# Kernel tuning notes

Hardware: AMD Instinct MI355X
Metric: run time of the kernel (lower is better)

The kernel has to match this reference:

```python
import jax, jax.numpy as jnp
import numpy as np

N_NODES = 100000
N_EDGES = 3200000
OUT_FEATURES = 128


def setup_inputs() -> dict:
    key = jax.random.key(0)
    k1, k2, k3, k4, k5 = jax.random.split(key, 5)
    edge_row = jax.random.randint(k1, (N_EDGES,), 0, N_NODES, dtype=jnp.int32)
    edge_col = jax.random.randint(k2, (N_EDGES,), 0, N_NODES, dtype=jnp.int32)
    edge_val = jax.random.uniform(k3, (N_EDGES,), dtype=jnp.float32)
    stdv = 1.0 / np.sqrt(OUT_FEATURES)
    weight = jax.random.uniform(k4, (N_NODES, OUT_FEATURES), minval=-stdv, maxval=stdv, dtype=jnp.float32)
    bias = jax.random.uniform(k5, (OUT_FEATURES,), minval=-stdv, maxval=stdv, dtype=jnp.float32)
    return {"edge_row": edge_row, "edge_col": edge_col, "edge_val": edge_val,
            "weight": weight, "bias": bias}


def reference(edge_row, edge_col, edge_val, weight, bias):
    # SpMM: out = adj @ weight, adj given in COO (row, col, val), shape [N, N]
    n_nodes = weight.shape[0]
    gathered = edge_val[:, None] * weight[edge_col]            # [E, F]
    out = jax.ops.segment_sum(gathered, edge_row, num_segments=n_nodes)  # [N, F]
    return out + bias
```

## Files before the change

### kernel.cpp

```cpp
#include <hip/hip_runtime.h>

#define F 128
#define RB 64
#define RB_SHIFT 6
#define CAP 4096
#define SCH 4096
#define PT3 1024
#define EPT3 (SCH / PT3)
#define NSEG 8
#define COL_BITS 17
#define COL_MASK 0x1FFFF
#define MAXNB 2048

__global__ __launch_bounds__(256) void cvt_chist_kernel(
    const float4* __restrict__ w4, uint* __restrict__ wq32, float* __restrict__ scales,
    int total4, const int* __restrict__ rows, int* __restrict__ cntmat, int n_edges,
    int nb, int nchunks) {
    if ((int)blockIdx.x < nchunks) {
        __shared__ int h[MAXNB];
        int c = blockIdx.x, t = threadIdx.x;
        for (int i = t; i < nb; i += 256) h[i] = 0;
        __syncthreads();
        int e0 = c * SCH, e1 = min(e0 + SCH, n_edges);
        if (e1 - e0 == SCH) {
            const int4* r4 = (const int4*)(rows + e0);
#pragma unroll
            for (int k = 0; k < 4; k++) {
                int4 rv = r4[k * 256 + t];
                atomicAdd(&h[rv.x >> RB_SHIFT], 1);
                atomicAdd(&h[rv.y >> RB_SHIFT], 1);
                atomicAdd(&h[rv.z >> RB_SHIFT], 1);
                atomicAdd(&h[rv.w >> RB_SHIFT], 1);
            }
        } else {
            for (int e = e0 + t; e < e1; e += 256) atomicAdd(&h[rows[e] >> RB_SHIFT], 1);
        }
        __syncthreads();
        for (int i = t; i < nb; i += 256) cntmat[(size_t)c * nb + i] = h[i];
    } else {
        int idx = (blockIdx.x - nchunks) * 256 + threadIdx.x;
        if (idx >= total4) return;
        float4 f = w4[idx];
        float m = fmaxf(fmaxf(fabsf(f.x), fabsf(f.y)), fmaxf(fabsf(f.z), fabsf(f.w)));
#pragma unroll
        for (int off = 1; off <= 16; off <<= 1) m = fmaxf(m, __shfl_xor(m, off));
        float inv = m > 0.f ? 127.f / m : 0.f;
        int q0 = (int)rintf(f.x * inv);
        int q1 = (int)rintf(f.y * inv);
        int q2 = (int)rintf(f.z * inv);
        int q3 = (int)rintf(f.w * inv);
        wq32[idx] = (q0 & 0xFF) | ((q1 & 0xFF) << 8) | ((q2 & 0xFF) << 16) |
                    ((q3 & 0xFF) << 24);
        if ((idx & 31) == 0) scales[idx >> 5] = m * (1.f / 127.f);
    }
}

__global__ __launch_bounds__(256) void scanA_kernel(int* __restrict__ cntmat,
                                                    int* __restrict__ segsum,
                                                    int nb, int nchunks) {
    int b = blockIdx.x * 256 + threadIdx.x;
    if (b >= nb) return;
    int sg = blockIdx.y;
    int cps = (nchunks + NSEG - 1) / NSEG;
    int c0 = sg * cps, c1 = min(c0 + cps, nchunks);
    int run = 0;
#pragma unroll 4
    for (int c = c0; c < c1; c++) {
        int v = cntmat[(size_t)c * nb + b];
        cntmat[(size_t)c * nb + b] = run;
        run += v;
    }
    segsum[sg * nb + b] = run;
}

__global__ void scanBC_kernel(int* __restrict__ segsum, int* __restrict__ boffs, int nb) {
    __shared__ int lds[1024];
    int t = threadIdx.x;
    int per = (nb + 1023) / 1024;
    int base = t * per;
    int cnt[2] = {0, 0};
    int s = 0;
    for (int i = 0; i < per && i < 2; i++) {
        int b = base + i;
        int run = 0;
        if (b < nb) {
            for (int sg = 0; sg < NSEG; sg++) {
                int v = segsum[sg * nb + b];
                segsum[sg * nb + b] = run;
                run += v;
            }
        }
        cnt[i] = run;
        s += run;
    }
    lds[t] = s;
    __syncthreads();
    for (int off = 1; off < 1024; off <<= 1) {
        int a = (t >= off) ? lds[t - off] : 0;
        __syncthreads();
        lds[t] += a;
        __syncthreads();
    }
    int excl = lds[t] - s;
    for (int i = 0; i < per && i < 2; i++) {
        int b = base + i;
        if (b < nb) {
            boffs[b] = excl;
            excl += cnt[i];
        }
    }
    if (t == 1023) boffs[nb] = lds[1023];
}

__global__ __launch_bounds__(PT3) void scatter_kernel(
    const int* __restrict__ rows, const int* __restrict__ cols,
    const float* __restrict__ vals, const float* __restrict__ scales,
    const int* __restrict__ boffs, const int* __restrict__ segsum,
    const int* __restrict__ cntmat, int2* __restrict__ epk, int n_edges, int nb,
    int nchunks) {
    __shared__ int relc[MAXNB];
    __shared__ int hist[MAXNB];
    __shared__ int lcur[MAXNB];
    __shared__ int2 buf[SCH];
    __shared__ ushort sbkt[SCH];
    __shared__ int wsum[PT3 / 64], wbase[PT3 / 64];
    int t = threadIdx.x;
    int lane = t & 63, w = t >> 6;
    int cps = (nchunks + NSEG - 1) / NSEG;
    int c = blockIdx.x;

    int e0 = c * SCH, e1 = min(e0 + SCH, n_edges);
    int cnt = e1 - e0;
    int sg = c / cps;

    for (int i = t; i < nb; i += PT3) {
        relc[i] = boffs[i] + segsum[sg * nb + i] + cntmat[(size_t)c * nb + i];
        hist[i] = 0;
    }
    __syncthreads();

    int er[EPT3], ec[EPT3];
    float ev[EPT3];
    int eb = e0 + (t << 2);
    if (eb + 4 <= e1) {
        int4 rv = *(const int4*)(rows + eb);
        int4 cv = *(const int4*)(cols + eb);
        float4 vv = *(const float4*)(vals + eb);
        er[0] = rv.x; er[1] = rv.y; er[2] = rv.z; er[3] = rv.w;
        ec[0] = cv.x; ec[1] = cv.y; ec[2] = cv.z; ec[3] = cv.w;
        ev[0] = vv.x * scales[ec[0]];
        ev[1] = vv.y * scales[ec[1]];
        ev[2] = vv.z * scales[ec[2]];
        ev[3] = vv.w * scales[ec[3]];
#pragma unroll
        for (int k = 0; k < 4; k++) atomicAdd(&hist[er[k] >> RB_SHIFT], 1);
    } else {
#pragma unroll
        for (int k = 0; k < 4; k++) {
            int e = eb + k;
            if (e < e1) {
                er[k] = rows[e];
                ec[k] = cols[e];
                ev[k] = vals[e] * scales[ec[k]];
                atomicAdd(&hist[er[k] >> RB_SHIFT], 1);
            }
        }
    }
    __syncthreads();

    int b0 = t << 1;
    int h0 = (b0 + 0 < nb) ? hist[b0 + 0] : 0;
    int h1 = (b0 + 1 < nb) ? hist[b0 + 1] : 0;
    int psum = h0 + h1;
    int v = psum;
#pragma unroll
    for (int off = 1; off < 64; off <<= 1) {
        int a = __shfl_up(v, off);
        if (lane >= off) v += a;
    }
    if (lane == 63) wsum[w] = v;
    __syncthreads();
    if (t == 0) {
        int run = 0;
        for (int i = 0; i < PT3 / 64; i++) {
            wbase[i] = run;
            run += wsum[i];
        }
    }
    __syncthreads();
    int excl = v - psum + wbase[w];
    if (b0 + 0 < nb) { lcur[b0 + 0] = excl; relc[b0 + 0] -= excl; }
    excl += h0;
    if (b0 + 1 < nb) { lcur[b0 + 1] = excl; relc[b0 + 1] -= excl; }
    __syncthreads();

#pragma unroll
    for (int k = 0; k < EPT3; k++) {
        int e = eb + k;
        if (e < e1) {
            int b = er[k] >> RB_SHIFT;
            int p = atomicAdd(&lcur[b], 1);
            buf[p] = make_int2(ec[k] | ((er[k] & (RB - 1)) << COL_BITS),
                               __float_as_int(ev[k]));
            sbkt[p] = (ushort)b;
        }
    }
    __syncthreads();

    for (int i = t; i < cnt; i += PT3) epk[relc[sbkt[i]] + i] = buf[i];
}

__global__ __launch_bounds__(512, 8) void sortacc_kernel(
    const int* __restrict__ boffs, const int2* __restrict__ epk,
    const ushort* __restrict__ wq, const float* __restrict__ bias,
    float* __restrict__ out, int n_nodes) {
    __shared__ int2 buf[CAP];
    __shared__ int hist[RB], lstart[RB], lcur[RB];
    int b = blockIdx.x;
    int s = boffs[b];
    int cnt = boffs[b + 1] - s;
    int row0 = b << RB_SHIFT;
    int t = threadIdx.x;
    int lane = t & 63, w = t >> 6;
    float2 bb = ((const float2*)bias)[lane];

#define DEQX(u) ((float)(int)(signed char)((u) & 0xFF))
#define DEQY(u) ((float)((int)(short)(u) >> 8))
#define WOFF(px) ((((uint)(px) & COL_MASK) << 6) | (uint)lane)

    if (cnt <= CAP) {
        if (t < RB) hist[t] = 0;
        __syncthreads();
        int2 r0, r1, r2, r3, r4, r5, r6, r7;
#define LOADK(rk, k)                                                     \
        {                                                                \
            int i = t + (k)*512;                                         \
            if (i < cnt) {                                               \
                rk = epk[s + i];                                         \
                atomicAdd(&hist[(unsigned)rk.x >> COL_BITS], 1);         \
            }                                                            \
        }
        LOADK(r0, 0) LOADK(r1, 1) LOADK(r2, 2) LOADK(r3, 3)
        LOADK(r4, 4) LOADK(r5, 5) LOADK(r6, 6) LOADK(r7, 7)
#undef LOADK
        __syncthreads();
        if (w == 0) {
            int hv = hist[lane];
            int v = hv;
#pragma unroll
            for (int off = 1; off < 64; off <<= 1) {
                int a = __shfl_up(v, off);
                if (lane >= off) v += a;
            }
            lstart[lane] = v - hv;
            lcur[lane] = v - hv;
        }
        __syncthreads();
#define SCATK(rk, k)                                                         \
        {                                                                    \
            int i = t + (k)*512;                                             \
            if (i < cnt) {                                                   \
                int p = atomicAdd(&lcur[(unsigned)rk.x >> COL_BITS], 1);     \
                buf[p] = make_int2((int)(((uint)rk.x & COL_MASK) << 6), rk.y);\
            }                                                                \
        }
        SCATK(r0, 0) SCATK(r1, 1) SCATK(r2, 2) SCATK(r3, 3)
        SCATK(r4, 4) SCATK(r5, 5) SCATK(r6, 6) SCATK(r7, 7)
#undef SCATK
        __syncthreads();

        for (int j = 0; j < 8; j++) {
            int rl = w * 8 + j;
            int gr = row0 + rl;
            if (gr >= n_nodes) break;
            int e = lstart[rl];
            int end = e + hist[rl];
            float ax = 0.f, ay = 0.f;
            for (; e + 12 <= end; e += 12) {
                int2 p0 = buf[e],     p1 = buf[e + 1], p2 = buf[e + 2];
                int2 p3 = buf[e + 3], p4 = buf[e + 4], p5 = buf[e + 5];
                int2 p6 = buf[e + 6], p7 = buf[e + 7], p8 = buf[e + 8];
                int2 p9 = buf[e + 9], pa = buf[e + 10], pb = buf[e + 11];
                uint u0 = wq[(uint)p0.x + lane];
                uint u1 = wq[(uint)p1.x + lane];
                uint u2 = wq[(uint)p2.x + lane];
                uint u3 = wq[(uint)p3.x + lane];
                uint u4 = wq[(uint)p4.x + lane];
                uint u5 = wq[(uint)p5.x + lane];
                uint u6 = wq[(uint)p6.x + lane];
                uint u7 = wq[(uint)p7.x + lane];
                uint u8 = wq[(uint)p8.x + lane];
                uint u9 = wq[(uint)p9.x + lane];
                uint ua = wq[(uint)pa.x + lane];
                uint ub = wq[(uint)pb.x + lane];
                float v0 = __int_as_float(p0.y), v1 = __int_as_float(p1.y);
                float v2 = __int_as_float(p2.y), v3 = __int_as_float(p3.y);
                float v4 = __int_as_float(p4.y), v5 = __int_as_float(p5.y);
                float v6 = __int_as_float(p6.y), v7 = __int_as_float(p7.y);
                float v8 = __int_as_float(p8.y), v9 = __int_as_float(p9.y);
                float va = __int_as_float(pa.y), vb = __int_as_float(pb.y);
                ax += v0 * DEQX(u0) + v1 * DEQX(u1) + v2 * DEQX(u2) + v3 * DEQX(u3) +
                      v4 * DEQX(u4) + v5 * DEQX(u5) + v6 * DEQX(u6) + v7 * DEQX(u7) +
                      v8 * DEQX(u8) + v9 * DEQX(u9) + va * DEQX(ua) + vb * DEQX(ub);
                ay += v0 * DEQY(u0) + v1 * DEQY(u1) + v2 * DEQY(u2) + v3 * DEQY(u3) +
                      v4 * DEQY(u4) + v5 * DEQY(u5) + v6 * DEQY(u6) + v7 * DEQY(u7) +
                      v8 * DEQY(u8) + v9 * DEQY(u9) + va * DEQY(ua) + vb * DEQY(ub);
            }
            for (; e + 4 <= end; e += 4) {
                int2 p0 = buf[e], p1 = buf[e + 1], p2 = buf[e + 2], p3 = buf[e + 3];
                uint u0 = wq[(uint)p0.x + lane];
                uint u1 = wq[(uint)p1.x + lane];
                uint u2 = wq[(uint)p2.x + lane];
                uint u3 = wq[(uint)p3.x + lane];
                float v0 = __int_as_float(p0.y), v1 = __int_as_float(p1.y);
                float v2 = __int_as_float(p2.y), v3 = __int_as_float(p3.y);
                ax += v0 * DEQX(u0) + v1 * DEQX(u1) + v2 * DEQX(u2) + v3 * DEQX(u3);
                ay += v0 * DEQY(u0) + v1 * DEQY(u1) + v2 * DEQY(u2) + v3 * DEQY(u3);
            }
            for (; e < end; ++e) {
                int2 pk = buf[e];
                uint u = wq[(uint)pk.x + lane];
                float v = __int_as_float(pk.y);
                ax += v * DEQX(u);
                ay += v * DEQY(u);
            }
            ((float2*)(out + (size_t)gr * F))[lane] = make_float2(ax + bb.x, ay + bb.y);
        }
    } else {
        for (int j = 0; j < 8; j++) {
            int rl = w * 8 + j;
            int gr = row0 + rl;
            if (gr >= n_nodes) break;
            float ax = 0.f, ay = 0.f;
            for (int e = s; e < s + cnt; ++e) {
                int2 pk = epk[e];
                if ((int)((unsigned)pk.x >> COL_BITS) == rl) {
                    uint u = wq[WOFF(pk.x)];
                    float v = __int_as_float(pk.y);
                    ax += v * DEQX(u);
                    ay += v * DEQY(u);
                }
            }
            ((float2*)(out + (size_t)gr * F))[lane] = make_float2(ax + bb.x, ay + bb.y);
        }
    }
#undef DEQX
#undef DEQY
#undef WOFF
}

__global__ void init_out_kernel(float* __restrict__ out, const float* __restrict__ bias,
                                int n_nodes) {
    const float4* b4 = (const float4*)bias;
    float4* o4 = (float4*)out;
    int total = n_nodes * (F / 4);
    for (int i = blockIdx.x * blockDim.x + threadIdx.x; i < total;
         i += gridDim.x * blockDim.x)
        o4[i] = b4[i & (F / 4 - 1)];
}

__global__ void edge_scatter_kernel(const int* __restrict__ rows,
                                    const int* __restrict__ cols,
                                    const float* __restrict__ vals,
                                    const float* __restrict__ weight,
                                    float* __restrict__ out, int n_edges) {
    int e = (blockIdx.x * blockDim.x + threadIdx.x) >> 6;
    if (e >= n_edges) return;
    int lane = threadIdx.x & 63;
    float2 w = ((const float2*)(weight + (size_t)cols[e] * F))[lane];
    float val = vals[e];
    float* o = out + (size_t)rows[e] * F + lane * 2;
    unsafeAtomicAdd(o, val * w.x);
    unsafeAtomicAdd(o + 1, val * w.y);
}

extern "C" void kernel_launch(void* const* d_in, const int* in_sizes, int n_in,
                              void* d_out, int out_size, void* d_ws, size_t ws_size,
                              hipStream_t stream) {
    const int*   rows   = (const int*)d_in[0];
    const int*   cols   = (const int*)d_in[1];
    const float* vals   = (const float*)d_in[2];
    const float* weight = (const float*)d_in[3];
    const float* bias   = (const float*)d_in[4];
    float* out = (float*)d_out;

    int n_edges = in_sizes[0];
    int n_nodes = out_size / F;
    int nb = (n_nodes + RB - 1) / RB;
    int nchunks = (n_edges + SCH - 1) / SCH;

    size_t head_ints  = ((size_t)nb + 2) & ~(size_t)1;
    size_t epk_off    = head_ints * 4;
    size_t scales_off = epk_off + (size_t)n_edges * 8;
    size_t wq_off     = (scales_off + (size_t)n_nodes * 4 + 255) & ~(size_t)255;
    size_t mat_off    = (wq_off + (size_t)n_nodes * F + 255) & ~(size_t)255;
    size_t seg_off    = mat_off + (size_t)nchunks * nb * 4;
    size_t need       = seg_off + (size_t)NSEG * nb * 4;

    if (ws_size < need || n_nodes > (1 << COL_BITS) || nb > MAXNB) {
        init_out_kernel<<<2048, 256, 0, stream>>>(out, bias, n_nodes);
        int grid = (n_edges + 3) / 4;
        edge_scatter_kernel<<<grid, 256, 0, stream>>>(rows, cols, vals, weight, out,
                                                      n_edges);
        return;
    }

    int* boffs    = (int*)d_ws;
    int2* epk     = (int2*)((char*)d_ws + epk_off);
    float* scales = (float*)((char*)d_ws + scales_off);
    ushort* wq    = (ushort*)((char*)d_ws + wq_off);
    int* cntmat   = (int*)((char*)d_ws + mat_off);
    int* segsum   = (int*)((char*)d_ws + seg_off);

    int total4 = n_nodes * (F / 4);
    int cvt_blocks = (total4 + 255) / 256;
    cvt_chist_kernel<<<nchunks + cvt_blocks, 256, 0, stream>>>(
        (const float4*)weight, (uint*)wq, scales, total4, rows, cntmat, n_edges, nb,
        nchunks);
    dim3 ga((nb + 255) / 256, NSEG);
    scanA_kernel<<<ga, 256, 0, stream>>>(cntmat, segsum, nb, nchunks);
    scanBC_kernel<<<1, 1024, 0, stream>>>(segsum, boffs, nb);
    scatter_kernel<<<nchunks, PT3, 0, stream>>>(rows, cols, vals, scales, boffs, segsum,
                                                cntmat, epk, n_edges, nb, nchunks);
    sortacc_kernel<<<nb, 512, 0, stream>>>(boffs, epk, wq, bias, out, n_nodes);
}
```

Before: 145.7 us.

## Fuse scan kernels via last-block arrival; offset-binary int8 gather with dual-edge lanes

The two scan passes are merged into one kernel, where the last block to arrive (detected with an atomic counter reset in the first kernel) runs the final cross-bucket scan. This removes one launch. The weights are quantised as offset-binary bytes (+128), and the row accumulation now has each half-wave process a different edge with 32-bit loads and 4 features per lane. The half-waves are combined with a shuffle, and the +128 bias is corrected using the sum of edge values. This doubles edge parallelism per wave and simplifies dequantisation, at the cost of extra shuffles and a numerical correction term.

```diff
diff --git a/kernel.cpp b/kernel.cpp
--- a/kernel.cpp
+++ b/kernel.cpp
@@ -15,7 +15,8 @@
 __global__ __launch_bounds__(256) void cvt_chist_kernel(
     const float4* __restrict__ w4, uint* __restrict__ wq32, float* __restrict__ scales,
     int total4, const int* __restrict__ rows, int* __restrict__ cntmat, int n_edges,
-    int nb, int nchunks) {
+    int nb, int nchunks, int* __restrict__ arrive) {
+    if (blockIdx.x == 0 && threadIdx.x == 0) *arrive = 0;
     if ((int)blockIdx.x < nchunks) {
         __shared__ int h[MAXNB];
         int c = blockIdx.x, t = threadIdx.x;
@@ -45,71 +46,76 @@
 #pragma unroll
         for (int off = 1; off <= 16; off <<= 1) m = fmaxf(m, __shfl_xor(m, off));
         float inv = m > 0.f ? 127.f / m : 0.f;
-        int q0 = (int)rintf(f.x * inv);
-        int q1 = (int)rintf(f.y * inv);
-        int q2 = (int)rintf(f.z * inv);
-        int q3 = (int)rintf(f.w * inv);
-        wq32[idx] = (q0 & 0xFF) | ((q1 & 0xFF) << 8) | ((q2 & 0xFF) << 16) |
-                    ((q3 & 0xFF) << 24);
+        int q0 = (int)rintf(f.x * inv) + 128;
+        int q1 = (int)rintf(f.y * inv) + 128;
+        int q2 = (int)rintf(f.z * inv) + 128;
+        int q3 = (int)rintf(f.w * inv) + 128;
+        wq32[idx] = (uint)(q0 | (q1 << 8) | (q2 << 16) | (q3 << 24));
         if ((idx & 31) == 0) scales[idx >> 5] = m * (1.f / 127.f);
     }
 }
 
-__global__ __launch_bounds__(256) void scanA_kernel(int* __restrict__ cntmat,
-                                                    int* __restrict__ segsum,
-                                                    int nb, int nchunks) {
+__global__ __launch_bounds__(256) void scan_fused_kernel(
+    int* __restrict__ cntmat, int* __restrict__ segsum, int* __restrict__ boffs,
+    int* __restrict__ arrive, int nb, int nchunks) {
     int b = blockIdx.x * 256 + threadIdx.x;
-    if (b >= nb) return;
     int sg = blockIdx.y;
     int cps = (nchunks + NSEG - 1) / NSEG;
-    int c0 = sg * cps, c1 = min(c0 + cps, nchunks);
-    int run = 0;
+    if (b < nb) {
+        int c0 = sg * cps, c1 = min(c0 + cps, nchunks);
+        int run = 0;
 #pragma unroll 4
-    for (int c = c0; c < c1; c++) {
-        int v = cntmat[(size_t)c * nb + b];
-        cntmat[(size_t)c * nb + b] = run;
-        run += v;
-    }
-    segsum[sg * nb + b] = run;
-}
-
-__global__ void scanBC_kernel(int* __restrict__ segsum, int* __restrict__ boffs, int nb) {
-    __shared__ int lds[1024];
+        for (int c = c0; c < c1; c++) {
+            int v = cntmat[(size_t)c * nb + b];
+            cntmat[(size_t)c * nb + b] = run;
+            run += v;
+        }
+        segsum[sg * nb + b] = run;
+    }
+    __threadfence();
+    __syncthreads();
+    __shared__ int lastflag;
+    if (threadIdx.x == 0)
+        lastflag = (atomicAdd(arrive, 1) == (int)(gridDim.x * gridDim.y) - 1);
+    __syncthreads();
+    if (!lastflag) return;
+    __threadfence();
+    __shared__ int lds[256];
     int t = threadIdx.x;
-    int per = (nb + 1023) / 1024;
+    int per = (nb + 255) / 256;
     int base = t * per;
-    int cnt[2] = {0, 0};
+    int cnts[8];
     int s = 0;
-    for (int i = 0; i < per && i < 2; i++) {
-        int b = base + i;
+    for (int i = 0; i < per && i < 8; i++) {
+        int bb = base + i;
         int run = 0;
-        if (b < nb) {
-            for (int sg = 0; sg < NSEG; sg++) {
-                int v = segsum[sg * nb + b];
-                segsum[sg * nb + b] = run;
+        if (bb < nb) {
+            for (int g = 0; g < NSEG; g++) {
+                int v = segsum[g * nb + bb];
+                segsum[g * nb + bb] = run;
                 run += v;
             }
         }
-        cnt[i] = run;
+        cnts[i] = run;
         s += run;
     }
     lds[t] = s;
     __syncthreads();
-    for (int off = 1; off < 1024; off <<= 1) {
+    for (int off = 1; off < 256; off <<= 1) {
         int a = (t >= off) ? lds[t - off] : 0;
         __syncthreads();
         lds[t] += a;
         __syncthreads();
     }
     int excl = lds[t] - s;
-    for (int i = 0; i < per && i < 2; i++) {
-        int b = base + i;
-        if (b < nb) {
-            boffs[b] = excl;
-            excl += cnt[i];
-        }
-    }
-    if (t == 1023) boffs[nb] = lds[1023];
+    for (int i = 0; i < per && i < 8; i++) {
+        int bb = base + i;
+        if (bb < nb) {
+            boffs[bb] = excl;
+            excl += cnts[i];
+        }
+    }
+    if (t == 255) boffs[nb] = lds[255];
 }
 
 __global__ __launch_bounds__(PT3) void scatter_kernel(
@@ -212,7 +218,7 @@
 
 __global__ __launch_bounds__(512, 8) void sortacc_kernel(
     const int* __restrict__ boffs, const int2* __restrict__ epk,
-    const ushort* __restrict__ wq, const float* __restrict__ bias,
+    const uint* __restrict__ wq32, const float* __restrict__ bias,
     float* __restrict__ out, int n_nodes) {
     __shared__ int2 buf[CAP];
     __shared__ int hist[RB], lstart[RB], lcur[RB];
@@ -222,11 +228,14 @@
     int row0 = b << RB_SHIFT;
     int t = threadIdx.x;
     int lane = t & 63, w = t >> 6;
-    float2 bb = ((const float2*)bias)[lane];
-
-#define DEQX(u) ((float)(int)(signed char)((u) & 0xFF))
-#define DEQY(u) ((float)((int)(short)(u) >> 8))
-#define WOFF(px) ((((uint)(px) & COL_MASK) << 6) | (uint)lane)
+    int half = lane >> 5;
+    int c32 = lane & 31;
+    float4 bb4 = ((const float4*)bias)[c32];
+
+#define B0(u) ((float)((u) & 0xFFu))
+#define B1(u) ((float)(((u) >> 8) & 0xFFu))
+#define B2(u) ((float)(((u) >> 16) & 0xFFu))
+#define B3(u) ((float)((u) >> 24))
 
     if (cnt <= CAP) {
         if (t < RB) hist[t] = 0;
@@ -261,7 +270,7 @@
             int i = t + (k)*512;                                             \
             if (i < cnt) {                                                   \
                 int p = atomicAdd(&lcur[(unsigned)rk.x >> COL_BITS], 1);     \
-                buf[p] = make_int2((int)(((uint)rk.x & COL_MASK) << 6), rk.y);\
+                buf[p] = make_int2((int)(((uint)rk.x & COL_MASK) << 5), rk.y);\
             }                                                                \
         }
         SCATK(r0, 0) SCATK(r1, 1) SCATK(r2, 2) SCATK(r3, 3)
@@ -275,78 +284,99 @@
             if (gr >= n_nodes) break;
             int e = lstart[rl];
             int end = e + hist[rl];
-            float ax = 0.f, ay = 0.f;
+            float ax0 = 0.f, ax1 = 0.f, ax2 = 0.f, ax3 = 0.f, sv = 0.f;
             for (; e + 12 <= end; e += 12) {
-                int2 p0 = buf[e],     p1 = buf[e + 1], p2 = buf[e + 2];
-                int2 p3 = buf[e + 3], p4 = buf[e + 4], p5 = buf[e + 5];
-                int2 p6 = buf[e + 6], p7 = buf[e + 7], p8 = buf[e + 8];
-                int2 p9 = buf[e + 9], pa = buf[e + 10], pb = buf[e + 11];
-                uint u0 = wq[(uint)p0.x + lane];
-                uint u1 = wq[(uint)p1.x + lane];
-                uint u2 = wq[(uint)p2.x + lane];
-                uint u3 = wq[(uint)p3.x + lane];
-                uint u4 = wq[(uint)p4.x + lane];
-                uint u5 = wq[(uint)p5.x + lane];
-                uint u6 = wq[(uint)p6.x + lane];
-                uint u7 = wq[(uint)p7.x + lane];
-                uint u8 = wq[(uint)p8.x + lane];
-                uint u9 = wq[(uint)p9.x + lane];
-                uint ua = wq[(uint)pa.x + lane];
-                uint ub = wq[(uint)pb.x + lane];
+                int2 p0 = buf[e + 0 + half], p1 = buf[e + 2 + half];
+                int2 p2 = buf[e + 4 + half], p3 = buf[e + 6 + half];
+                int2 p4 = buf[e + 8 + half], p5 = buf[e + 10 + half];
+                uint u0 = wq32[(uint)p0.x + c32];
+                uint u1 = wq32[(uint)p1.x + c32];
+                uint u2 = wq32[(uint)p2.x + c32];
+                uint u3 = wq32[(uint)p3.x + c32];
+                uint u4 = wq32[(uint)p4.x + c32];
+                uint u5 = wq32[(uint)p5.x + c32];
                 float v0 = __int_as_float(p0.y), v1 = __int_as_float(p1.y);
                 float v2 = __int_as_float(p2.y), v3 = __int_as_float(p3.y);
                 float v4 = __int_as_float(p4.y), v5 = __int_as_float(p5.y);
-                float v6 = __int_as_float(p6.y), v7 = __int_as_float(p7.y);
-                float v8 = __int_as_float(p8.y), v9 = __int_as_float(p9.y);
-                float va = __int_as_float(pa.y), vb = __int_as_float(pb.y);
-                ax += v0 * DEQX(u0) + v1 * DEQX(u1) + v2 * DEQX(u2) + v3 * DEQX(u3) +
-                      v4 * DEQX(u4) + v5 * DEQX(u5) + v6 * DEQX(u6) + v7 * DEQX(u7) +
-                      v8 * DEQX(u8) + v9 * DEQX(u9) + va * DEQX(ua) + vb * DEQX(ub);
-                ay += v0 * DEQY(u0) + v1 * DEQY(u1) + v2 * DEQY(u2) + v3 * DEQY(u3) +
-                      v4 * DEQY(u4) + v5 * DEQY(u5) + v6 * DEQY(u6) + v7 * DEQY(u7) +
-                      v8 * DEQY(u8) + v9 * DEQY(u9) + va * DEQY(ua) + vb * DEQY(ub);
-            }
-            for (; e + 4 <= end; e += 4) {
-                int2 p0 = buf[e], p1 = buf[e + 1], p2 = buf[e + 2], p3 = buf[e + 3];
-                uint u0 = wq[(uint)p0.x + lane];
-                uint u1 = wq[(uint)p1.x + lane];
-                uint u2 = wq[(uint)p2.x + lane];
-                uint u3 = wq[(uint)p3.x + lane];
-                float v0 = __int_as_float(p0.y), v1 = __int_as_float(p1.y);
-                float v2 = __int_as_float(p2.y), v3 = __int_as_float(p3.y);
-                ax += v0 * DEQX(u0) + v1 * DEQX(u1) + v2 * DEQX(u2) + v3 * DEQX(u3);
-                ay += v0 * DEQY(u0) + v1 * DEQY(u1) + v2 * DEQY(u2) + v3 * DEQY(u3);
-            }
-            for (; e < end; ++e) {
+                ax0 += v0 * B0(u0) + v1 * B0(u1) + v2 * B0(u2) + v3 * B0(u3) +
+                       v4 * B0(u4) + v5 * B0(u5);
+                ax1 += v0 * B1(u0) + v1 * B1(u1) + v2 * B1(u2) + v3 * B1(u3) +
+                       v4 * B1(u4) + v5 * B1(u5);
+                ax2 += v0 * B2(u0) + v1 * B2(u1) + v2 * B2(u2) + v3 * B2(u3) +
+                       v4 * B2(u4) + v5 * B2(u5);
+                ax3 += v0 * B3(u0) + v1 * B3(u1) + v2 * B3(u2) + v3 * B3(u3) +
+                       v4 * B3(u4) + v5 * B3(u5);
+                sv += ((v0 + v1) + (v2 + v3)) + (v4 + v5);
+            }
+            for (; e + 2 <= end; e += 2) {
+                int2 pk = buf[e + half];
+                uint u = wq32[(uint)pk.x + c32];
+                float v = __int_as_float(pk.y);
+                ax0 += v * B0(u);
+                ax1 += v * B1(u);
+                ax2 += v * B2(u);
+                ax3 += v * B3(u);
+                sv += v;
+            }
+            if (e < end && half == 0) {
                 int2 pk = buf[e];
-                uint u = wq[(uint)pk.x + lane];
+                uint u = wq32[(uint)pk.x + c32];
                 float v = __int_as_float(pk.y);
-                ax += v * DEQX(u);
-                ay += v * DEQY(u);
-            }
-            ((float2*)(out + (size_t)gr * F))[lane] = make_float2(ax + bb.x, ay + bb.y);
+                ax0 += v * B0(u);
+                ax1 += v * B1(u);
+                ax2 += v * B2(u);
+                ax3 += v * B3(u);
+                sv += v;
+            }
+            ax0 += __shfl_xor(ax0, 32);
+            ax1 += __shfl_xor(ax1, 32);
+            ax2 += __shfl_xor(ax2, 32);
+            ax3 += __shfl_xor(ax3, 32);
+            sv += __shfl_xor(sv, 32);
+            if (half == 0) {
+                float corr = 128.f * sv;
+                ((float4*)out)[(size_t)gr * 32 + c32] =
+                    make_float4(ax0 - corr + bb4.x, ax1 - corr + bb4.y,
+                                ax2 - corr + bb4.z, ax3 - corr + bb4.w);
+            }
         }
     } else {
         for (int j = 0; j < 8; j++) {
             int rl = w * 8 + j;
             int gr = row0 + rl;
             if (gr >= n_nodes) break;
-            float ax = 0.f, ay = 0.f;
-            for (int e = s; e < s + cnt; ++e) {
-                int2 pk = epk[e];
-                if ((int)((unsigned)pk.x >> COL_BITS) == rl) {
-                    uint u = wq[WOFF(pk.x)];
-                    float v = __int_as_float(pk.y);
-                    ax += v * DEQX(u);
-                    ay += v * DEQY(u);
+            float ax0 = 0.f, ax1 = 0.f, ax2 = 0.f, ax3 = 0.f, sv = 0.f;
+            if (half == 0) {
+                for (int e = s; e < s + cnt; ++e) {
+                    int2 pk = epk[e];
+                    if ((int)((unsigned)pk.x >> COL_BITS) == rl) {
+                        uint u = wq32[(((uint)pk.x & COL_MASK) << 5) + c32];
+                        float v = __int_as_float(pk.y);
+                        ax0 += v * B0(u);
+                        ax1 += v * B1(u);
+                        ax2 += v * B2(u);
+                        ax3 += v * B3(u);
+                        sv += v;
+                    }
                 }
             }
-            ((float2*)(out + (size_t)gr * F))[lane] = make_float2(ax + bb.x, ay + bb.y);
-        }
-    }
-#undef DEQX
-#undef DEQY
-#undef WOFF
+            ax0 += __shfl_xor(ax0, 32);
+            ax1 += __shfl_xor(ax1, 32);
+            ax2 += __shfl_xor(ax2, 32);
+            ax3 += __shfl_xor(ax3, 32);
+            sv += __shfl_xor(sv, 32);
+            if (half == 0) {
+                float corr = 128.f * sv;
+                ((float4*)out)[(size_t)gr * 32 + c32] =
+                    make_float4(ax0 - corr + bb4.x, ax1 - corr + bb4.y,
+                                ax2 - corr + bb4.z, ax3 - corr + bb4.w);
+            }
+        }
+    }
+#undef B0
+#undef B1
+#undef B2
+#undef B3
 }
 
 __global__ void init_out_kernel(float* __restrict__ out, const float* __restrict__ bias,
@@ -395,7 +425,8 @@
     size_t wq_off     = (scales_off + (size_t)n_nodes * 4 + 255) & ~(size_t)255;
     size_t mat_off    = (wq_off + (size_t)n_nodes * F + 255) & ~(size_t)255;
     size_t seg_off    = mat_off + (size_t)nchunks * nb * 4;
-    size_t need       = seg_off + (size_t)NSEG * nb * 4;
+    size_t arr_off    = seg_off + (size_t)NSEG * nb * 4;
+    size_t need       = arr_off + 16;
 
     if (ws_size < need || n_nodes > (1 << COL_BITS) || nb > MAXNB) {
         init_out_kernel<<<2048, 256, 0, stream>>>(out, bias, n_nodes);
@@ -408,19 +439,19 @@
     int* boffs    = (int*)d_ws;
     int2* epk     = (int2*)((char*)d_ws + epk_off);
     float* scales = (float*)((char*)d_ws + scales_off);
-    ushort* wq    = (ushort*)((char*)d_ws + wq_off);
+    uint* wq32    = (uint*)((char*)d_ws + wq_off);
     int* cntmat   = (int*)((char*)d_ws + mat_off);
     int* segsum   = (int*)((char*)d_ws + seg_off);
+    int* arrive   = (int*)((char*)d_ws + arr_off);
 
     int total4 = n_nodes * (F / 4);
     int cvt_blocks = (total4 + 255) / 256;
     cvt_chist_kernel<<<nchunks + cvt_blocks, 256, 0, stream>>>(
-        (const float4*)weight, (uint*)wq, scales, total4, rows, cntmat, n_edges, nb,
-        nchunks);
+        (const float4*)weight, wq32, scales, total4, rows, cntmat, n_edges, nb, nchunks,
+        arrive);
     dim3 ga((nb + 255) / 256, NSEG);
-    scanA_kernel<<<ga, 256, 0, stream>>>(cntmat, segsum, nb, nchunks);
-    scanBC_kernel<<<1, 1024, 0, stream>>>(segsum, boffs, nb);
+    scan_fused_kernel<<<ga, 256, 0, stream>>>(cntmat, segsum, boffs, arrive, nb, nchunks);
     scatter_kernel<<<nchunks, PT3, 0, stream>>>(rows, cols, vals, scales, boffs, segsum,
                                                 cntmat, epk, n_edges, nb, nchunks);
-    sortacc_kernel<<<nb, 512, 0, stream>>>(boffs, epk, wq, bias, out, n_nodes);
-}
+    sortacc_kernel<<<nb, 512, 0, stream>>>(boffs, epk, wq32, bias, out, n_nodes);
+}
```

Measured after the change: 153.1 us. 1.05x slower.
